# Kernel optimization log

Hardware: AMD Instinct MI355X
Metric: run time of the kernel (lower is better)

The kernel has to match this reference:

```python
import jax, jax.numpy as jnp
import numpy as np

B, T, V, E, H = 64, 512, 8192, 1024, 2048


def setup_inputs() -> dict:
    key = jax.random.key(0)
    k = jax.random.split(key, 8)
    idx = jax.random.randint(k[0], (B, T), 0, V)
    targets = jax.random.randint(k[1], (B, T), 0, V)
    s = 0.02
    W_E = jax.random.normal(k[2], (V, E), jnp.float32) * s
    start = jnp.zeros((1, H), jnp.float32)
    W_xh = jax.random.normal(k[3], (E + H, H), jnp.float32) * s  # Linear(E+H -> H)
    b_xh = jnp.zeros((H,), jnp.float32)
    W_head = jax.random.normal(k[4], (H, V), jnp.float32) * s
    b_head = jnp.zeros((V,), jnp.float32)
    return {"idx": idx, "targets": targets, "W_E": W_E, "start": start,
            "W_xh": W_xh, "b_xh": b_xh, "W_head": W_head, "b_head": b_head}


def reference(idx, targets, W_E, start, W_xh, b_xh, W_head, b_head):
    b, t = idx.shape
    emb = W_E[idx]  # [B, T, E]
    # split concat-linear: cat([x,h]) @ W_xh == x @ Wx + h @ Wh (same math)
    Wx, Wh = W_xh[:E], W_xh[E:]
    xproj = jnp.einsum('bte,eh->bth', emb, Wx) + b_xh  # precompute input part

    def step(h_prev, xp_t):
        h_t = jnp.tanh(xp_t + h_prev @ Wh)
        return h_t, h_t

    h0 = jnp.broadcast_to(start, (b, H))
    _, hs = jax.lax.scan(step, h0, jnp.swapaxes(xproj, 0, 1))  # [T, B, H]
    hidden = jnp.swapaxes(hs, 0, 1)  # [B, T, H]
    logits = jnp.einsum('bth,hv->btv', hidden, W_head) + b_head

    # cross entropy with ignore_index=-1
    logp = jax.nn.log_softmax(logits, axis=-1)
    mask = targets != -1
    tsafe = jnp.where(mask, targets, 0)
    nll = -jnp.take_along_axis(logp, tsafe[..., None], axis=-1)[..., 0]
    loss = jnp.sum(nll * mask) / jnp.maximum(jnp.sum(mask), 1)
    return logits, loss
```

## Files before the change

kernel.cpp:

```cpp
#include <hip/hip_runtime.h>
#include <hip/hip_bf16.h>
#include <math.h>
#include <stdint.h>

#define Bb 64
#define Tt 512
#define Vv 8192
#define Ee 1024
#define Hh 2048

typedef unsigned short u16;
typedef unsigned long long u64;
typedef __attribute__((ext_vector_type(8))) short bf16x8;
typedef __attribute__((ext_vector_type(8))) _Float16 f16x8;
typedef __attribute__((ext_vector_type(4))) float f32x4;

__device__ __forceinline__ u16 f2b(float f) {
  unsigned u = __float_as_uint(f);
  u += 0x7FFF + ((u >> 16) & 1);
  return (u16)(u >> 16);
}
__device__ __forceinline__ float b2f(u16 h) {
  return __uint_as_float(((unsigned)h) << 16);
}
__device__ __forceinline__ u16 f2h_bits(float f) {
  union { _Float16 h; u16 u; } c;
  c.h = (_Float16)f;
  return c.u;
}

__device__ __forceinline__ void gload16f(f16x8& dst, const void* addr) {
  asm volatile("global_load_dwordx4 %0, %1, off sc1"
               : "=v"(dst) : "v"(addr) : "memory");
}
__device__ __forceinline__ void gstore2_sc1(void* addr, unsigned val) {
  asm volatile("global_store_short %0, %1, off sc1"
               :: "v"(addr), "v"(val) : "memory");
}

__device__ __forceinline__ void gll16(const u16* g, const u16* l) {
  __builtin_amdgcn_global_load_lds((__attribute__((address_space(1))) void*)g,
                                   (__attribute__((address_space(3))) void*)l, 16, 0, 0);
}

__device__ __forceinline__ float wave_max(float v) {
  #pragma unroll
  for (int d = 32; d; d >>= 1) v = fmaxf(v, __shfl_xor(v, d, 64));
  return v;
}
__device__ __forceinline__ float wave_sum(float v) {
  #pragma unroll
  for (int d = 32; d; d >>= 1) v += __shfl_xor(v, d, 64);
  return v;
}


__global__ __launch_bounds__(256)
void embed_cast_f16(const float* __restrict__ WE, const int* __restrict__ idx,
                    u16* __restrict__ emb) {
  const int m = blockIdx.x;
  const int row = idx[m];
  const float4 v = ((const float4*)(WE + (size_t)row * Ee))[threadIdx.x];
  ushort4 o;
  o.x = f2h_bits(v.x); o.y = f2h_bits(v.y);
  o.z = f2h_bits(v.z); o.w = f2h_bits(v.w);
  ((ushort4*)(emb + (size_t)m * Ee))[threadIdx.x] = o;
}

__global__ __launch_bounds__(256)
void transpose_cast_f16(const float* __restrict__ src, u16* __restrict__ dst,
                        int R, int C) {
  __shared__ float tile[32][33];
  const int bi = blockIdx.x;
  const int bj = blockIdx.y;
  const int tid = threadIdx.x;
  const int r  = tid >> 3;
  const int c4 = (tid & 7) * 4;
  float4 v = *(const float4*)(src + (size_t)(bj * 32 + r) * C + bi * 32 + c4);
  tile[r][c4 + 0] = v.x; tile[r][c4 + 1] = v.y;
  tile[r][c4 + 2] = v.z; tile[r][c4 + 3] = v.w;
  __syncthreads();
  ushort4 o;
  o.x = f2h_bits(tile[c4 + 0][r]); o.y = f2h_bits(tile[c4 + 1][r]);
  o.z = f2h_bits(tile[c4 + 2][r]); o.w = f2h_bits(tile[c4 + 3][r]);
  *(ushort4*)(dst + (size_t)(bi * 32 + r) * R + bj * 32 + c4) = o;
}

__global__ __launch_bounds__(256)
void h0_init(const float* __restrict__ start, u16* __restrict__ hbuf) {
  const int b = blockIdx.x;
  #pragma unroll
  for (int j = 0; j < 8; ++j) {
    int n = threadIdx.x * 8 + j;
    hbuf[(size_t)b * 2048 + n] = f2h_bits(start[n]);
  }
}

template <int MODE, int F16>
__global__ __launch_bounds__(256, 2)
void gemm_bt(const u16* __restrict__ A, const u16* __restrict__ Bt,
             const float* __restrict__ bias, void* __restrict__ outp,
             float* __restrict__ pm, float* __restrict__ ps,
             int M, int N, int K) {
  __shared__ u16 ldsA[128 * 32];
  __shared__ u16 ldsB[128 * 32];
  __shared__ float sm_[2][2][64];
  __shared__ float ss_[2][2][64];
  const int tid = threadIdx.x;
  const int lane = tid & 63;
  const int w = tid >> 6;
  const int wr = w >> 1, wc = w & 1;

  const int nwg = gridDim.x * gridDim.y;
  const int lin = blockIdx.y * gridDim.x + blockIdx.x;
  const int swz = (lin & 7) * (nwg >> 3) + (lin >> 3);
  const int bm = swz % gridDim.x;
  const int bn = swz / gridDim.x;

  const int srow = w * 32 + (lane >> 2);
  const int scol = (lane & 3) * 8;
  const u16* a0 = A + (size_t)(bm * 128 + srow) * K + scol;
  const u16* b0 = Bt + (size_t)(bn * 128 + srow) * K + scol;
  u16* lA0 = ldsA + w * 1024;
  u16* lA1 = ldsA + w * 1024 + 512;
  u16* lB0 = ldsB + w * 1024;
  u16* lB1 = ldsB + w * 1024 + 512;

  f32x4 acc[4][4];
  #pragma unroll
  for (int m = 0; m < 4; ++m)
    #pragma unroll
    for (int n = 0; n < 4; ++n)
      acc[m][n] = (f32x4){0.f, 0.f, 0.f, 0.f};

  const int nk = K >> 5;
  for (int kt = 0; kt < nk; ++kt) {
    __syncthreads();
    const u16* ak = a0 + kt * 32;
    const u16* bk = b0 + kt * 32;
    gll16(ak, lA0);
    gll16(ak + 16 * (size_t)K, lA1);
    gll16(bk, lB0);
    gll16(bk + 16 * (size_t)K, lB1);
    __syncthreads();
    bf16x8 af[4], bfr[4];
    #pragma unroll
    for (int i = 0; i < 4; ++i) {
      af[i]  = *(const bf16x8*)&ldsA[(wr * 64 + i * 16 + (lane & 15)) * 32 + (lane >> 4) * 8];
      bfr[i] = *(const bf16x8*)&ldsB[(wc * 64 + i * 16 + (lane & 15)) * 32 + (lane >> 4) * 8];
    }
    #pragma unroll
    for (int m = 0; m < 4; ++m)
      #pragma unroll
      for (int n = 0; n < 4; ++n) {
        if (F16) {
          acc[m][n] = __builtin_amdgcn_mfma_f32_16x16x32_f16(
              *(const f16x8*)&af[m], *(const f16x8*)&bfr[n], acc[m][n], 0, 0, 0);
        } else {
          acc[m][n] = __builtin_amdgcn_mfma_f32_16x16x32_bf16(af[m], bfr[n], acc[m][n], 0, 0, 0);
        }
      }
  }

  const int r0 = bm * 128 + wr * 64 + (lane >> 4) * 4;
  const int c0 = bn * 128 + wc * 64 + (lane & 15);

  if (MODE == 0) {
    float bv[4];
    #pragma unroll
    for (int n = 0; n < 4; ++n) bv[n] = bias[c0 + n * 16];
    #pragma unroll
    for (int m = 0; m < 4; ++m) {
      #pragma unroll
      for (int q = 0; q < 4; ++q) {
        const int row = r0 + m * 16 + q;
        float v[4];
        float mx = -1e30f;
        #pragma unroll
        for (int n = 0; n < 4; ++n) {
          v[n] = acc[m][n][q] + bv[n];
          ((float*)outp)[(size_t)row * N + c0 + n * 16] = v[n];
          mx = fmaxf(mx, v[n]);
        }
        #pragma unroll
        for (int d = 1; d < 16; d <<= 1) mx = fmaxf(mx, __shfl_xor(mx, d, 64));
        float se = 0.f;
        #pragma unroll
        for (int n = 0; n < 4; ++n) se += expf(v[n] - mx);
        #pragma unroll
        for (int d = 1; d < 16; d <<= 1) se += __shfl_xor(se, d, 64);
        if ((lane & 15) == 0) {
          const int rl = m * 16 + (lane >> 4) * 4 + q;
          sm_[wc][wr][rl] = mx;
          ss_[wc][wr][rl] = se;
        }
      }
    }
    __syncthreads();
    if (w < 2) {
      float m0 = sm_[0][w][lane], m1 = sm_[1][w][lane];
      float s0 = ss_[0][w][lane], s1 = ss_[1][w][lane];
      float Mx = fmaxf(m0, m1);
      float S = s0 * expf(m0 - Mx) + s1 * expf(m1 - Mx);
      const int row = bm * 128 + w * 64 + lane;
      pm[(size_t)row * 64 + bn] = Mx;
      ps[(size_t)row * 64 + bn] = S;
    }
  } else {
    #pragma unroll
    for (int n = 0; n < 4; ++n) {
      const int col = c0 + n * 16;
      const float bv = bias[col];
      #pragma unroll
      for (int m = 0; m < 4; ++m) {
        #pragma unroll
        for (int q = 0; q < 4; ++q) {
          const int row = r0 + m * 16 + q;
          float v = acc[m][n][q] + bv;
          const int b = row >> 9, t = row & 511;
          ((u16*)outp)[((size_t)t * Bb + b) * N + col] = f2b(v);
        }
      }
    }
  }
}

__global__ __launch_bounds__(512, 2)
void rnn_scan(const u16* __restrict__ WhT, const u16* __restrict__ xp,
              u16* __restrict__ hbuf, u16* __restrict__ hidden,
              unsigned* __restrict__ sync) {
  __shared__ u16 whi[65536];
  __shared__ float red[4096];

  const int bid = blockIdx.x;
  const int g = bid >> 6;
  const int colg = bid & 63;
  const int rowbase = g * 16;
  const int col0 = colg * 32;
  const int tid = threadIdx.x;
  const int lane = tid & 63;
  const int w = tid >> 6;

  for (int i = tid; i < 8192; i += 512) {
    const int ch = i & 3;
    const int cl = (i >> 2) & 15;
    const int kt = (i >> 6) & 63;
    const int c2 = (i >> 12) & 1;
    bf16x8 v = *(const bf16x8*)(WhT + (size_t)(col0 + c2 * 16 + cl) * 2048 + kt * 32 + ch * 8);
    *(bf16x8*)&whi[(size_t)(c2 * 64 + kt) * 512 + ch * 128 + cl * 8] = v;
  }
  __syncthreads();

  unsigned* cnt = sync + g * 64;
  bool dead = false;
  const int hrow = rowbase + (lane & 15);

  const int ev = w * 64 + lane;
  const int ef = ev >> 8;
  const int ep = ev & 255;
  const int el = ep >> 2, eq = ep & 3;
  const int erow = rowbase + (el & 15);
  const int ecol = col0 + ef * 16 + ((el >> 4) << 2) + eq;

  u16 xv16 = xp[(size_t)erow * 2048 + ecol];

  for (int t = 0; t < Tt; ++t) {
    const u16* hp = hbuf + (size_t)(t & 1) * (64 * 2048);
    u16*       hn = hbuf + (size_t)((t + 1) & 1) * (64 * 2048);

    f16x8 qh[8];
    const u16* hb = hp + (size_t)hrow * 2048 + (lane >> 4) * 8;
    #pragma unroll
    for (int kt = 0; kt < 8; ++kt)
      gload16f(qh[kt], hb + (w * 8 + kt) * 32);
    asm volatile("s_waitcnt vmcnt(0)" ::: "memory");
    __builtin_amdgcn_sched_barrier(0);

    f32x4 a0 = (f32x4){0.f, 0.f, 0.f, 0.f};
    f32x4 a1 = (f32x4){0.f, 0.f, 0.f, 0.f};
    #pragma unroll
    for (int kt = 0; kt < 8; ++kt) {
      const int ktG = w * 8 + kt;
      f16x8 w0 = *(const f16x8*)&whi[(size_t)(0 * 64 + ktG) * 512 + (lane >> 4) * 128 + (lane & 15) * 8];
      f16x8 w1 = *(const f16x8*)&whi[(size_t)(1 * 64 + ktG) * 512 + (lane >> 4) * 128 + (lane & 15) * 8];
      a0 = __builtin_amdgcn_mfma_f32_16x16x32_f16(w0, qh[kt], a0, 0, 0, 0);
      a1 = __builtin_amdgcn_mfma_f32_16x16x32_f16(w1, qh[kt], a1, 0, 0, 0);
    }

    *(f32x4*)&red[(w) * 256 + lane * 4]     = a0;
    *(f32x4*)&red[(8 + w) * 256 + lane * 4] = a1;
    __syncthreads();

    {
      float s = 0.f;
      #pragma unroll
      for (int j = 0; j < 8; ++j)
        s += red[(ef * 8 + j) * 256 + ep];
      float hv = tanhf(s + b2f(xv16));
      u16 hf = f2h_bits(hv);
      gstore2_sc1(hn + (size_t)erow * 2048 + ecol, (unsigned)hf);
      hidden[((size_t)erow * Tt + t) * Hh + ecol] = hf;
    }

    __syncthreads();
    if (t + 1 < Tt)
      xv16 = xp[((size_t)(t + 1) * Bb + erow) * 2048 + ecol];
    if (tid == 0) {
      unsigned old = __hip_atomic_fetch_add(cnt, 1u, __ATOMIC_RELAXED, __HIP_MEMORY_SCOPE_AGENT);
      if (old != (unsigned)(t * 64 + 63) && !dead) {
        unsigned polls = 0;
        while (__hip_atomic_load(cnt, __ATOMIC_RELAXED, __HIP_MEMORY_SCOPE_AGENT)
               < (unsigned)((t + 1) * 64)) {
          __builtin_amdgcn_s_sleep(1);
          if (++polls > 1000000u) { dead = true; break; }
        }
      }
    }
    __syncthreads();
  }
}


__global__ __launch_bounds__(256)
void nll_from_partials(const float* __restrict__ pm, const float* __restrict__ ps,
                       const float* __restrict__ logits, const int* __restrict__ tgt,
                       float* __restrict__ nll) {
  const int r = blockIdx.x * 4 + (threadIdx.x >> 6);
  const int lane = threadIdx.x & 63;
  float m = pm[(size_t)r * 64 + lane];
  float s = ps[(size_t)r * 64 + lane];
  float M = wave_max(m);
  float S = wave_sum(s * expf(m - M));
  if (lane == 0) {
    const int tg = tgt[r];
    float o = 0.f;
    if (tg != -1) o = M + logf(S) - logits[(size_t)r * Vv + tg];
    nll[r] = o;
  }
}

__global__ __launch_bounds__(256)
void loss_reduce(const float* __restrict__ nll, const int* __restrict__ tgt,
                 float* __restrict__ out) {
  const int tid = threadIdx.x;
  float s = 0.f, c = 0.f;
  for (int i = tid; i < Bb * Tt; i += 256) {
    s += nll[i];
    c += (tgt[i] != -1) ? 1.f : 0.f;
  }
  s = wave_sum(s);
  c = wave_sum(c);
  __shared__ float as_[4], ac_[4];
  const int w = tid >> 6;
  if ((tid & 63) == 0) { as_[w] = s; ac_[w] = c; }
  __syncthreads();
  if (tid == 0) {
    float S = as_[0] + as_[1] + as_[2] + as_[3];
    float C = ac_[0] + ac_[1] + ac_[2] + ac_[3];
    out[0] = S / fmaxf(C, 1.f);
  }
}


extern "C" void kernel_launch(void* const* d_in, const int* in_sizes, int n_in,
                              void* d_out, int out_size, void* d_ws, size_t ws_size,
                              hipStream_t stream) {
  const int*   idx    = (const int*)d_in[0];
  const int*   tgt    = (const int*)d_in[1];
  const float* W_E    = (const float*)d_in[2];
  const float* start  = (const float*)d_in[3];
  const float* W_xh   = (const float*)d_in[4];
  const float* b_xh   = (const float*)d_in[5];
  const float* W_head = (const float*)d_in[6];
  const float* b_head = (const float*)d_in[7];

  char* ws = (char*)d_ws;
  u16*      emb16  = (u16*)(ws);
  u16*      hidden = (u16*)(ws);
  u16*      xproj  = (u16*)(ws + (size_t)128 * 1024 * 1024);
  float*    pm     = (float*)(ws + (size_t)128 * 1024 * 1024);
  float*    ps     = (float*)(ws + (size_t)136 * 1024 * 1024);
  u16*      WheadT = (u16*)(ws + (size_t)256 * 1024 * 1024);
  u16*      WhT    = (u16*)(ws + (size_t)288 * 1024 * 1024);
  u16*      WxT16  = (u16*)(ws + (size_t)304 * 1024 * 1024);
  u16*      hbuf   = (u16*)(ws + (size_t)312 * 1024 * 1024);
  float*    nll    = (float*)(ws + (size_t)313 * 1024 * 1024);
  unsigned* sync   = (unsigned*)(ws + (size_t)313 * 1024 * 1024 + 128 * 1024);

  embed_cast_f16<<<Bb * Tt, 256, 0, stream>>>(W_E, idx, emb16);
  transpose_cast_f16<<<dim3(Hh / 32, Ee / 32), 256, 0, stream>>>(W_xh, WxT16, Ee, Hh);
  transpose_cast_f16<<<dim3(Hh / 32, Hh / 32), 256, 0, stream>>>(W_xh + (size_t)Ee * Hh, WhT, Hh, Hh);
  transpose_cast_f16<<<dim3(Vv / 32, Hh / 32), 256, 0, stream>>>(W_head, WheadT, Hh, Vv);
  h0_init<<<Bb, 256, 0, stream>>>(start, hbuf);
  hipMemsetAsync(sync, 0, 1024, stream);

  gemm_bt<1, 1><<<dim3(256, 16), 256, 0, stream>>>(emb16, WxT16, b_xh, xproj, nullptr, nullptr,
                                                   Bb * Tt, Hh, 1024);

  rnn_scan<<<256, 512, 0, stream>>>(WhT, xproj, hbuf, hidden, sync);

  gemm_bt<0, 1><<<dim3(256, 64), 256, 0, stream>>>(hidden, WheadT, b_head, d_out, pm, ps,
                                                   Bb * Tt, Vv, 2048);

  nll_from_partials<<<Bb * Tt / 4, 256, 0, stream>>>(pm, ps, (const float*)d_out, tgt, nll);
  loss_reduce<<<1, 256, 0, stream>>>(nll, tgt, (float*)d_out + ((size_t)out_size - 1));
}
```

Baseline: 4.391 ms.

## Replace 128x128 GEMM with 256x256 tile, 4-stage LDS pipeline and 8 waves

Swaps the simple single-buffered 128x128 bf16/f16 GEMM for a 256x256 tile kernel with 512 threads. It stages four K-slices in 128KB of LDS, prefetches three ahead and interleaves global-to-LDS loads with MFMA halves using barriers and setprio. The aim is to hide global-load latency and raise data reuse per tile for both the input-projection and head GEMMs. The softmax partials now come from 32 column blocks instead of 64, so the NLL kernel is changed to match. The large LDS footprint limits occupancy, and the hand-written waitcnt counts must stay consistent with the number of loads in flight.

After: 4.172 ms. 5.0% less time.

```diff
diff --git a/kernel.cpp b/kernel.cpp
--- a/kernel.cpp
+++ b/kernel.cpp
@@ -97,132 +97,173 @@
 }
 
 template <int MODE, int F16>
-__global__ __launch_bounds__(256, 2)
-void gemm_bt(const u16* __restrict__ A, const u16* __restrict__ Bt,
+__global__ __launch_bounds__(512, 2)
+void gemm256(const u16* __restrict__ A, const u16* __restrict__ Bt,
              const float* __restrict__ bias, void* __restrict__ outp,
              float* __restrict__ pm, float* __restrict__ ps,
              int M, int N, int K) {
-  __shared__ u16 ldsA[128 * 32];
-  __shared__ u16 ldsB[128 * 32];
-  __shared__ float sm_[2][2][64];
-  __shared__ float ss_[2][2][64];
+  __shared__ u16 lds[65536];
+
   const int tid = threadIdx.x;
   const int lane = tid & 63;
   const int w = tid >> 6;
-  const int wr = w >> 1, wc = w & 1;
+  const int wm = w >> 2;
+  const int wn = w & 3;
+  const int l15 = lane & 15, l16 = lane >> 4;
 
   const int nwg = gridDim.x * gridDim.y;
   const int lin = blockIdx.y * gridDim.x + blockIdx.x;
   const int swz = (lin & 7) * (nwg >> 3) + (lin >> 3);
   const int bm = swz % gridDim.x;
   const int bn = swz / gridDim.x;
-
-  const int srow = w * 32 + (lane >> 2);
-  const int scol = (lane & 3) * 8;
-  const u16* a0 = A + (size_t)(bm * 128 + srow) * K + scol;
-  const u16* b0 = Bt + (size_t)(bn * 128 + srow) * K + scol;
-  u16* lA0 = ldsA + w * 1024;
-  u16* lA1 = ldsA + w * 1024 + 512;
-  u16* lB0 = ldsB + w * 1024;
-  u16* lB1 = ldsB + w * 1024 + 512;
-
-  f32x4 acc[4][4];
+  const int bm256 = bm * 256, bn256 = bn * 256;
+
+  const size_t srcLane = (size_t)l15 * K + l16 * 8;
+  #define STG(P, R0, kt, base)                                                 \
+    {                                                                          \
+      gll16((P) + (size_t)((R0) + w * 16) * K + (size_t)(kt) * 32 + srcLane,   \
+            &lds[(base) + w * 512]);                                           \
+      gll16((P) + (size_t)((R0) + (8 + w) * 16) * K + (size_t)(kt) * 32 + srcLane, \
+            &lds[(base) + (8 + w) * 512]);                                     \
+    }
+  #define DSF(base, rbase) \
+    (*(const bf16x8*)&lds[(base) + ((rbase) >> 4) * 512 + l16 * 128 + l15 * 8])
+  #define MM1(a, b, c)                                                          \
+    (F16 ? __builtin_amdgcn_mfma_f32_16x16x32_f16(*(const f16x8*)&(a),          \
+                                                  *(const f16x8*)&(b), (c), 0, 0, 0) \
+         : __builtin_amdgcn_mfma_f32_16x16x32_bf16((a), (b), (c), 0, 0, 0))
+
+  f32x4 acc[8][4];
   #pragma unroll
-  for (int m = 0; m < 4; ++m)
+  for (int m = 0; m < 8; ++m)
     #pragma unroll
     for (int n = 0; n < 4; ++n)
       acc[m][n] = (f32x4){0.f, 0.f, 0.f, 0.f};
 
-  const int nk = K >> 5;
-  for (int kt = 0; kt < nk; ++kt) {
-    __syncthreads();
-    const u16* ak = a0 + kt * 32;
-    const u16* bk = b0 + kt * 32;
-    gll16(ak, lA0);
-    gll16(ak + 16 * (size_t)K, lA1);
-    gll16(bk, lB0);
-    gll16(bk + 16 * (size_t)K, lB1);
-    __syncthreads();
-    bf16x8 af[4], bfr[4];
-    #pragma unroll
-    for (int i = 0; i < 4; ++i) {
-      af[i]  = *(const bf16x8*)&ldsA[(wr * 64 + i * 16 + (lane & 15)) * 32 + (lane >> 4) * 8];
-      bfr[i] = *(const bf16x8*)&ldsB[(wc * 64 + i * 16 + (lane & 15)) * 32 + (lane >> 4) * 8];
-    }
-    #pragma unroll
-    for (int m = 0; m < 4; ++m)
+  const int NT = K >> 5;
+
+  for (int pt = 0; pt < 3; ++pt) {
+    STG(A,  bm256, pt, pt * 8192);
+    STG(Bt, bn256, pt, 32768 + pt * 8192);
+  }
+  asm volatile("s_waitcnt vmcnt(0)" ::: "memory");
+  __builtin_amdgcn_s_barrier();
+
+  for (int t = 0; t < NT; ++t) {
+    const int abase = (t & 3) * 8192;
+    const int bbase = 32768 + (t & 3) * 8192;
+    const int sb = (t + 3) & 3;
+    const bool stg = (t + 3 < NT);
+    bf16x8 aR[4], bR[4];
+
+    #pragma unroll
+    for (int j = 0; j < 4; ++j) bR[j] = DSF(bbase, wn * 64 + j * 16);
+    #pragma unroll
+    for (int i = 0; i < 4; ++i) aR[i] = DSF(abase, wm * 128 + i * 16);
+    if (stg) {
+      STG(A, bm256, t + 3, sb * 8192);
+      asm volatile("s_waitcnt vmcnt(8)" ::: "memory");
+    } else {
+      asm volatile("s_waitcnt vmcnt(0)" ::: "memory");
+    }
+    __builtin_amdgcn_s_barrier();
+    asm volatile("s_waitcnt lgkmcnt(0)" ::: "memory");
+    __builtin_amdgcn_sched_barrier(0);
+    __builtin_amdgcn_s_setprio(1);
+    #pragma unroll
+    for (int i = 0; i < 4; ++i)
       #pragma unroll
-      for (int n = 0; n < 4; ++n) {
-        if (F16) {
-          acc[m][n] = __builtin_amdgcn_mfma_f32_16x16x32_f16(
-              *(const f16x8*)&af[m], *(const f16x8*)&bfr[n], acc[m][n], 0, 0, 0);
-        } else {
-          acc[m][n] = __builtin_amdgcn_mfma_f32_16x16x32_bf16(af[m], bfr[n], acc[m][n], 0, 0, 0);
+      for (int j = 0; j < 4; ++j)
+        acc[i][j] = MM1(aR[i], bR[j], acc[i][j]);
+    __builtin_amdgcn_s_setprio(0);
+    __builtin_amdgcn_s_barrier();
+
+    #pragma unroll
+    for (int i = 0; i < 4; ++i) aR[i] = DSF(abase, wm * 128 + 64 + i * 16);
+    if (stg) {
+      STG(Bt, bn256, t + 3, 32768 + sb * 8192);
+      asm volatile("s_waitcnt vmcnt(8)" ::: "memory");
+    } else {
+      asm volatile("s_waitcnt vmcnt(0)" ::: "memory");
+    }
+    __builtin_amdgcn_s_barrier();
+    asm volatile("s_waitcnt lgkmcnt(0)" ::: "memory");
+    __builtin_amdgcn_sched_barrier(0);
+    __builtin_amdgcn_s_setprio(1);
+    #pragma unroll
+    for (int i = 0; i < 4; ++i)
+      #pragma unroll
+      for (int j = 0; j < 4; ++j)
+        acc[4 + i][j] = MM1(aR[i], bR[j], acc[4 + i][j]);
+    __builtin_amdgcn_s_setprio(0);
+    __builtin_amdgcn_s_barrier();
+  }
+
+  const int c0 = bn256 + wn * 64 + l15;
+  float bv[4];
+  #pragma unroll
+  for (int j = 0; j < 4; ++j) bv[j] = bias[c0 + j * 16];
+
+  if (MODE == 0) {
+    float* scr = (float*)lds;
+    float* outf = (float*)outp;
+    #pragma unroll
+    for (int fm = 0; fm < 8; ++fm) {
+      #pragma unroll
+      for (int q = 0; q < 4; ++q) {
+        const int rl = wm * 128 + (fm >> 2) * 64 + (fm & 3) * 16 + l16 * 4 + q;
+        const int row = bm256 + rl;
+        float v0 = acc[fm][0][q] + bv[0];
+        float v1 = acc[fm][1][q] + bv[1];
+        float v2 = acc[fm][2][q] + bv[2];
+        float v3 = acc[fm][3][q] + bv[3];
+        outf[(size_t)row * N + c0]      = v0;
+        outf[(size_t)row * N + c0 + 16] = v1;
+        outf[(size_t)row * N + c0 + 32] = v2;
+        outf[(size_t)row * N + c0 + 48] = v3;
+        float mx = fmaxf(fmaxf(v0, v1), fmaxf(v2, v3));
+        #pragma unroll
+        for (int d = 1; d < 16; d <<= 1) mx = fmaxf(mx, __shfl_xor(mx, d, 64));
+        float se = expf(v0 - mx) + expf(v1 - mx) + expf(v2 - mx) + expf(v3 - mx);
+        #pragma unroll
+        for (int d = 1; d < 16; d <<= 1) se += __shfl_xor(se, d, 64);
+        if (l15 == 0) {
+          scr[wn * 256 + rl] = mx;
+          scr[1024 + wn * 256 + rl] = se;
         }
       }
-  }
-
-  const int r0 = bm * 128 + wr * 64 + (lane >> 4) * 4;
-  const int c0 = bn * 128 + wc * 64 + (lane & 15);
-
-  if (MODE == 0) {
-    float bv[4];
-    #pragma unroll
-    for (int n = 0; n < 4; ++n) bv[n] = bias[c0 + n * 16];
-    #pragma unroll
-    for (int m = 0; m < 4; ++m) {
+    }
+    __syncthreads();
+    if (lane < 32) {
+      const int rl = w * 32 + lane;
+      float m0 = scr[rl], m1 = scr[256 + rl], m2 = scr[512 + rl], m3 = scr[768 + rl];
+      float Mx = fmaxf(fmaxf(m0, m1), fmaxf(m2, m3));
+      float S = scr[1024 + rl] * expf(m0 - Mx) + scr[1280 + rl] * expf(m1 - Mx)
+              + scr[1536 + rl] * expf(m2 - Mx) + scr[1792 + rl] * expf(m3 - Mx);
+      const int row = bm256 + rl;
+      const int nbn = N >> 8;
+      pm[(size_t)row * nbn + bn] = Mx;
+      ps[(size_t)row * nbn + bn] = S;
+    }
+  } else {
+    u16* outh = (u16*)outp;
+    #pragma unroll
+    for (int fm = 0; fm < 8; ++fm) {
       #pragma unroll
       for (int q = 0; q < 4; ++q) {
-        const int row = r0 + m * 16 + q;
-        float v[4];
-        float mx = -1e30f;
-        #pragma unroll
-        for (int n = 0; n < 4; ++n) {
-          v[n] = acc[m][n][q] + bv[n];
-          ((float*)outp)[(size_t)row * N + c0 + n * 16] = v[n];
-          mx = fmaxf(mx, v[n]);
-        }
-        #pragma unroll
-        for (int d = 1; d < 16; d <<= 1) mx = fmaxf(mx, __shfl_xor(mx, d, 64));
-        float se = 0.f;
-        #pragma unroll
-        for (int n = 0; n < 4; ++n) se += expf(v[n] - mx);
-        #pragma unroll
-        for (int d = 1; d < 16; d <<= 1) se += __shfl_xor(se, d, 64);
-        if ((lane & 15) == 0) {
-          const int rl = m * 16 + (lane >> 4) * 4 + q;
-          sm_[wc][wr][rl] = mx;
-          ss_[wc][wr][rl] = se;
-        }
+        const int row = bm256 + wm * 128 + (fm >> 2) * 64 + (fm & 3) * 16 + l16 * 4 + q;
+        const int b = row >> 9, t = row & 511;
+        u16* dst = outh + ((size_t)t * Bb + b) * N + c0;
+        dst[0]  = f2b(acc[fm][0][q] + bv[0]);
+        dst[16] = f2b(acc[fm][1][q] + bv[1]);
+        dst[32] = f2b(acc[fm][2][q] + bv[2]);
+        dst[48] = f2b(acc[fm][3][q] + bv[3]);
       }
     }
-    __syncthreads();
-    if (w < 2) {
-      float m0 = sm_[0][w][lane], m1 = sm_[1][w][lane];
-      float s0 = ss_[0][w][lane], s1 = ss_[1][w][lane];
-      float Mx = fmaxf(m0, m1);
-      float S = s0 * expf(m0 - Mx) + s1 * expf(m1 - Mx);
-      const int row = bm * 128 + w * 64 + lane;
-      pm[(size_t)row * 64 + bn] = Mx;
-      ps[(size_t)row * 64 + bn] = S;
-    }
-  } else {
-    #pragma unroll
-    for (int n = 0; n < 4; ++n) {
-      const int col = c0 + n * 16;
-      const float bv = bias[col];
-      #pragma unroll
-      for (int m = 0; m < 4; ++m) {
-        #pragma unroll
-        for (int q = 0; q < 4; ++q) {
-          const int row = r0 + m * 16 + q;
-          float v = acc[m][n][q] + bv;
-          const int b = row >> 9, t = row & 511;
-          ((u16*)outp)[((size_t)t * Bb + b) * N + col] = f2b(v);
-        }
-      }
-    }
-  }
+  }
+  #undef STG
+  #undef DSF
+  #undef MM1
 }
 
 __global__ __launch_bounds__(512, 2)
@@ -327,8 +368,8 @@
                        float* __restrict__ nll) {
   const int r = blockIdx.x * 4 + (threadIdx.x >> 6);
   const int lane = threadIdx.x & 63;
-  float m = pm[(size_t)r * 64 + lane];
-  float s = ps[(size_t)r * 64 + lane];
+  float m = (lane < 32) ? pm[(size_t)r * 32 + lane] : -1e30f;
+  float s = (lane < 32) ? ps[(size_t)r * 32 + lane] : 0.f;
   float M = wave_max(m);
   float S = wave_sum(s * expf(m - M));
   if (lane == 0) {
@@ -394,12 +435,12 @@
   h0_init<<<Bb, 256, 0, stream>>>(start, hbuf);
   hipMemsetAsync(sync, 0, 1024, stream);
 
-  gemm_bt<1, 1><<<dim3(256, 16), 256, 0, stream>>>(emb16, WxT16, b_xh, xproj, nullptr, nullptr,
-                                                   Bb * Tt, Hh, 1024);
+  gemm256<1, 1><<<dim3(128, 8), 512, 0, stream>>>(emb16, WxT16, b_xh, xproj, nullptr, nullptr,
+                                                  Bb * Tt, Hh, 1024);
 
   rnn_scan<<<256, 512, 0, stream>>>(WhT, xproj, hbuf, hidden, sync);
 
-  gemm_bt<0, 1><<<dim3(256, 64), 256, 0, stream>>>(hidden, WheadT, b_head, d_out, pm, ps,
+  gemm256<0, 1><<<dim3(128, 32), 512, 0, stream>>>(hidden, WheadT, b_head, d_out, pm, ps,
                                                    Bb * Tt, Vv, 2048);
 
   nll_from_partials<<<Bb * Tt / 4, 256, 0, stream>>>(pm, ps, (const float*)d_out, tgt, nll);
```
